# Performance work log

Hardware: AMD Instinct MI355X
Metric: run time of the kernel (lower is better)

## Reference

```python
import jax, jax.numpy as jnp
import numpy as np

B, S, D_MODEL = 2, 2048, 1024
H, D = 16, 64
D_INNER = H * D
EPS = 1e-5


def setup_inputs() -> dict:
    key = jax.random.key(0)
    ks = jax.random.split(key, 10)
    sc = 0.02
    return {
        "x": jax.random.normal(ks[0], (B, S, D_MODEL), dtype=jnp.float32),
        "Wq": jax.random.normal(ks[1], (D_MODEL, D_INNER), dtype=jnp.float32) * sc,
        "Wk": jax.random.normal(ks[2], (D_MODEL, D_INNER), dtype=jnp.float32) * sc,
        "Wv": jax.random.normal(ks[3], (D_MODEL, D_INNER), dtype=jnp.float32) * sc,
        "Wg": jax.random.normal(ks[4], (D_MODEL, D_INNER), dtype=jnp.float32) * sc,
        "Wa": jax.random.normal(ks[5], (D_MODEL, H), dtype=jnp.float32) * sc,
        "ba": jax.random.normal(ks[6], (H,), dtype=jnp.float32) * sc,
        "Wo": jax.random.normal(ks[7], (D_INNER, D_MODEL), dtype=jnp.float32) * sc,
        "gn_w": jnp.ones((D_INNER,), dtype=jnp.float32),
        "gn_b": jnp.zeros((D_INNER,), dtype=jnp.float32),
    }


def reference(x, Wq, Wk, Wv, Wg, Wa, ba, Wo, gn_w, gn_b):
    b, s, _ = x.shape
    # projections -> [B,H,S,D]
    q = jax.nn.silu(jnp.einsum('bsm,md->bsd', x, Wq).reshape(b, s, H, D).transpose(0, 2, 1, 3))
    k = jax.nn.silu(jnp.einsum('bsm,md->bsd', x, Wk).reshape(b, s, H, D).transpose(0, 2, 1, 3))
    v = jnp.einsum('bsm,md->bsd', x, Wv).reshape(b, s, H, D).transpose(0, 2, 1, 3)

    # data-dependent log forget gate, per head: [B,H,S]
    log_alpha = -jax.nn.softplus(jnp.einsum('bsm,mh->bsh', x, Wa) + ba)
    cum = jnp.cumsum(log_alpha, axis=1).transpose(0, 2, 1)  # [B,H,S]

    # decay[b,h,i,j] = exp(cum[i] - cum[j]) for j <= i, else 0
    diff = cum[:, :, :, None] - cum[:, :, None, :]  # [B,H,S,S]
    causal = jnp.tril(jnp.ones((s, s), dtype=bool))
    decay = jnp.exp(jnp.where(causal, diff, -jnp.inf))

    attn = jnp.einsum('bhid,bhjd->bhij', q, k) * decay
    o = jnp.einsum('bhij,bhjd->bhid', attn, v)  # [B,H,S,D]
    o = o.transpose(0, 2, 1, 3)  # [B,S,H,D]

    # GroupNorm(H groups) over channels-within-group and spatial dim S
    mean = jnp.mean(o, axis=(1, 3), keepdims=True)          # per (b,h)
    var = jnp.var(o, axis=(1, 3), keepdims=True)
    o = (o - mean) / jnp.sqrt(var + EPS)
    o = o * gn_w.reshape(H, D) + gn_b.reshape(H, D)
    o = o.reshape(b, s, H * D)

    gate = jax.nn.sigmoid(jnp.einsum('bsm,md->bsd', x, Wg))
    return jnp.einsum('bsd,dm->bsm', o * gate, Wo)
```

## Files before the change

kernel.cpp:

```cpp
#include <hip/hip_runtime.h>
#include <math.h>
#include <stdint.h>

typedef __attribute__((ext_vector_type(4))) float f32x4;
typedef __attribute__((ext_vector_type(8))) short bf16x8;

constexpr int NB = 2;
constexpr int NS = 2048;
constexpr int NM = 1024;
constexpr int NH = 16;
constexpr int ND = 64;
constexpr int NDI = 1024;

__device__ __forceinline__ float bf2f(unsigned short u) {
  uint32_t x = ((uint32_t)u) << 16; float f; __builtin_memcpy(&f, &x, 4); return f;
}
__device__ __forceinline__ unsigned short f2bf(float f) {
  uint32_t x; __builtin_memcpy(&x, &f, 4);
  x += 0x7FFFu + ((x >> 16) & 1u);
  return (unsigned short)(x >> 16);
}

__global__ __launch_bounds__(256) void k_cast_bf16(const float* __restrict__ in,
    unsigned short* __restrict__ out, int n8) {
  int i = blockIdx.x * 256 + threadIdx.x;
  if (i >= n8) return;
  const float4* p = (const float4*)(in + (size_t)i * 8);
  float4 a = p[0], b = p[1];
  unsigned short r[8] = {f2bf(a.x), f2bf(a.y), f2bf(a.z), f2bf(a.w),
                         f2bf(b.x), f2bf(b.y), f2bf(b.z), f2bf(b.w)};
  *(uint4*)(out + (size_t)i * 8) = *(const uint4*)r;
}

__global__ __launch_bounds__(256) void k_castT5(
    const float* __restrict__ w0, const float* __restrict__ w1,
    const float* __restrict__ w2, const float* __restrict__ w3,
    const float* __restrict__ w4,
    unsigned short* __restrict__ t0, unsigned short* __restrict__ t1,
    unsigned short* __restrict__ t2, unsigned short* __restrict__ t3,
    unsigned short* __restrict__ t4) {
  __shared__ float tile[32][33];
  int z = blockIdx.z;
  const float* src = z == 0 ? w0 : z == 1 ? w1 : z == 2 ? w2 : z == 3 ? w3 : w4;
  unsigned short* dst = z == 0 ? t0 : z == 1 ? t1 : z == 2 ? t2 : z == 3 ? t3 : t4;
  int c0 = blockIdx.x * 32, r0 = blockIdx.y * 32;
  int tx = threadIdx.x & 31, ty = threadIdx.x >> 5;
  #pragma unroll
  for (int i = 0; i < 4; i++)
    tile[ty + i * 8][tx] = src[(size_t)(r0 + ty + i * 8) * 1024 + c0 + tx];
  __syncthreads();
  #pragma unroll
  for (int i = 0; i < 4; i++)
    dst[(size_t)(c0 + ty + i * 8) * 1024 + r0 + tx] = f2bf(tile[tx][ty + i * 8]);
}

__global__ __launch_bounds__(256) void k_wa_fill(const float* __restrict__ Wa,
    unsigned short* __restrict__ wa_pad) {
  int idx = blockIdx.x * 256 + threadIdx.x;
  int h = idx >> 10, k2 = idx & 1023;
  wa_pad[idx] = (h < 16) ? f2bf(Wa[k2 * 16 + h]) : (unsigned short)0;
}

__global__ __launch_bounds__(256) void k_la_gemm(const unsigned short* __restrict__ xb,
    const unsigned short* __restrict__ wa_pad, float* __restrict__ la4) {
  __shared__ unsigned short As[128 * 32];
  __shared__ unsigned short Bs[128 * 32];
  int tid = threadIdx.x;
  int row0 = blockIdx.y * 128;
  int kbeg = blockIdx.x * 256;
  float* Cp = la4 + (size_t)blockIdx.x * (32 * 2048);
  int w = tid >> 6, l = tid & 63;
  int wr = w >> 1, wc = w & 1;
  int lr = l & 15, lk = l >> 4;
  f32x4 acc[4] = {};
  for (int k0 = kbeg; k0 < kbeg + 256; k0 += 32) {
    __syncthreads();
    #pragma unroll
    for (int i = 0; i < 2; i++) {
      int idx = tid + i * 256;
      int r = idx >> 2, c = idx & 3;
      int cs = c ^ ((r >> 1) & 3);
      const unsigned short* srcA = xb + (size_t)(row0 + r) * NM + k0 + cs * 8;
      const unsigned short* srcB = wa_pad + (size_t)r * NM + k0 + cs * 8;
      __builtin_amdgcn_global_load_lds(
          (const __attribute__((address_space(1))) void*)srcA,
          (__attribute__((address_space(3))) void*)((char*)As + (w * 64 + i * 256) * 16),
          16, 0, 0);
      __builtin_amdgcn_global_load_lds(
          (const __attribute__((address_space(1))) void*)srcB,
          (__attribute__((address_space(3))) void*)((char*)Bs + (w * 64 + i * 256) * 16),
          16, 0, 0);
    }
    __syncthreads();
    if (wc == 0) {
      bf16x8 b = *(const bf16x8*)&Bs[lr * 32 + (lk ^ ((lr >> 1) & 3)) * 8];
      #pragma unroll
      for (int m = 0; m < 4; m++) {
        int ra = wr * 64 + m * 16 + lr;
        bf16x8 a = *(const bf16x8*)&As[ra * 32 + (lk ^ ((ra >> 1) & 3)) * 8];
        acc[m] = __builtin_amdgcn_mfma_f32_16x16x32_bf16(a, b, acc[m], 0, 0, 0);
      }
    }
  }
  if (wc == 0) {
    #pragma unroll
    for (int m = 0; m < 4; m++) {
      #pragma unroll
      for (int j = 0; j < 4; j++) {
        int row = row0 + wr * 64 + m * 16 + lk * 4 + j;
        int bb = row >> 11, s = row & 2047;
        Cp[((size_t)(bb * 16 + lr)) * 2048 + s] = acc[m][j];
      }
    }
  }
}

__global__ __launch_bounds__(256) void k_cumsum(const float* __restrict__ la4,
    const float* __restrict__ ba, float* __restrict__ cum,
    float* __restrict__ psum, float* __restrict__ psq) {
  int g = blockIdx.x;
  int h = g & 15;
  if (threadIdx.x == 0) { psum[g] = 0.f; psq[g] = 0.f; }
  float bah = ba[h];
  const float* p0 = la4 + (size_t)g * NS;
  float* out = cum + (size_t)g * NS;
  __shared__ float part[256];
  float v[8]; float sum = 0.f;
  int base = threadIdx.x * 8;
  #pragma unroll
  for (int i = 0; i < 8; i++) {
    int s = base + i;
    float z = p0[s] + p0[65536 + s] + p0[131072 + s] + p0[196608 + s] + bah;
    float sp = fmaxf(z, 0.f) + log1pf(expf(-fabsf(z)));
    v[i] = -sp; sum += v[i];
  }
  part[threadIdx.x] = sum;
  __syncthreads();
  for (int off = 1; off < 256; off <<= 1) {
    float add = (threadIdx.x >= off) ? part[threadIdx.x - off] : 0.f;
    __syncthreads();
    part[threadIdx.x] += add;
    __syncthreads();
  }
  float run = (threadIdx.x > 0) ? part[threadIdx.x - 1] : 0.f;
  #pragma unroll
  for (int i = 0; i < 8; i++) { run += v[i]; out[base + i] = run; }
}

__global__ __launch_bounds__(512, 2) void k_proj8(
    const unsigned short* __restrict__ A,
    const unsigned short* __restrict__ Wcat,
    unsigned short* __restrict__ q, unsigned short* __restrict__ k,
    unsigned short* __restrict__ v, unsigned short* __restrict__ g) {
  __shared__ unsigned short Ab[2][256 * 64];
  __shared__ unsigned short Bb[2][256 * 64];
  int tid = threadIdx.x;
  int bid = blockIdx.x;
  int wg = (bid & 7) * 32 + (bid >> 3);
  int bx = wg & 15, by = wg >> 4;
  int row0 = by * 256, col0 = bx * 256;
  int wid = tid >> 6, lane = tid & 63;
  int WR = wid >> 2, WC = wid & 3;
  int lr = lane & 15, lk = lane >> 4;

  auto stage = [&](int kt, int bi) {
    #pragma unroll
    for (int i = 0; i < 4; i++) {
      int idx = tid + i * 512;
      int r = idx >> 3, c = idx & 7;
      int cs = c ^ (r & 7);
      const unsigned short* srcA = A + (size_t)(row0 + r) * NM + kt * 64 + cs * 8;
      __builtin_amdgcn_global_load_lds(
          (const __attribute__((address_space(1))) void*)srcA,
          (__attribute__((address_space(3))) void*)((char*)&Ab[bi][0] + (wid * 64 + i * 512) * 16),
          16, 0, 0);
      const unsigned short* srcB = Wcat + (size_t)(col0 + r) * NM + kt * 64 + cs * 8;
      __builtin_amdgcn_global_load_lds(
          (const __attribute__((address_space(1))) void*)srcB,
          (__attribute__((address_space(3))) void*)((char*)&Bb[bi][0] + (wid * 64 + i * 512) * 16),
          16, 0, 0);
    }
  };

  stage(0, 0);
  stage(1, 1);

  f32x4 acc[8][4] = {};
  for (int kt = 0; kt < 16; ++kt) {
    int bi = kt & 1;
    if (kt < 15) asm volatile("s_waitcnt vmcnt(8)" ::: "memory");
    else         asm volatile("s_waitcnt vmcnt(0)" ::: "memory");
    __builtin_amdgcn_sched_barrier(0);
    __builtin_amdgcn_s_barrier();

    const char* Ap = (const char*)&Ab[bi][0];
    const char* Bp = (const char*)&Bb[bi][0];
    bf16x8 a0[8], b0[4], a1[8], b1[4];
    #pragma unroll
    for (int m = 0; m < 8; m++) {
      int r = WR * 128 + m * 16 + lr;
      a0[m] = *(const bf16x8*)(Ap + r * 128 + ((lk ^ (r & 7)) * 16));
    }
    #pragma unroll
    for (int n = 0; n < 4; n++) {
      int r = WC * 64 + n * 16 + lr;
      b0[n] = *(const bf16x8*)(Bp + r * 128 + ((lk ^ (r & 7)) * 16));
    }
    #pragma unroll
    for (int m = 0; m < 8; m++)
      #pragma unroll
      for (int n = 0; n < 4; n++)
        acc[m][n] = __builtin_amdgcn_mfma_f32_16x16x32_bf16(a0[m], b0[n], acc[m][n], 0, 0, 0);
    #pragma unroll
    for (int m = 0; m < 8; m++) {
      int r = WR * 128 + m * 16 + lr;
      a1[m] = *(const bf16x8*)(Ap + r * 128 + (((lk + 4) ^ (r & 7)) * 16));
    }
    #pragma unroll
    for (int n = 0; n < 4; n++) {
      int r = WC * 64 + n * 16 + lr;
      b1[n] = *(const bf16x8*)(Bp + r * 128 + (((lk + 4) ^ (r & 7)) * 16));
    }
    asm volatile("s_waitcnt lgkmcnt(0)" ::: "memory");
    __builtin_amdgcn_sched_barrier(0);
    __builtin_amdgcn_s_barrier();
    if (kt + 2 < 16) stage(kt + 2, bi);
    __builtin_amdgcn_s_setprio(1);
    #pragma unroll
    for (int m = 0; m < 8; m++)
      #pragma unroll
      for (int n = 0; n < 4; n++)
        acc[m][n] = __builtin_amdgcn_mfma_f32_16x16x32_bf16(a1[m], b1[n], acc[m][n], 0, 0, 0);
    __builtin_amdgcn_s_setprio(0);
  }

  #pragma unroll
  for (int m = 0; m < 8; m++) {
    #pragma unroll
    for (int n = 0; n < 4; n++) {
      int col = col0 + WC * 64 + n * 16 + lr;
      int zone = col >> 10;
      unsigned short* dst = zone == 0 ? q : zone == 1 ? k : zone == 2 ? v : g;
      int cb = col & 1023;
      #pragma unroll
      for (int j = 0; j < 4; j++) {
        int row = row0 + WR * 128 + m * 16 + lk * 4 + j;
        float val = acc[m][n][j];
        if (zone <= 1) val = val / (1.f + expf(-val));
        else if (zone == 3) val = 1.f / (1.f + expf(-val));
        dst[(size_t)row * 1024 + cb] = f2bf(val);
      }
    }
  }
}

__global__ __launch_bounds__(256) void k_out2(const unsigned short* __restrict__ A,
    const unsigned short* __restrict__ Bt, float* __restrict__ C) {
  __shared__ unsigned short As[2][128 * 64];
  __shared__ unsigned short Bs[2][128 * 64];
  int tid = threadIdx.x;
  int bid = blockIdx.x;
  int wg = (bid & 7) * 32 + (bid >> 3);
  int bx = wg & 7, by = wg >> 3;
  int row0 = by * 128, col0 = bx * 128;
  int w = tid >> 6, l = tid & 63;
  int wr = w >> 1, wc = w & 1;
  int lr = l & 15, lk = l >> 4;

  auto stage = [&](int t, int bi) {
    #pragma unroll
    for (int i = 0; i < 4; i++) {
      int idx = tid + i * 256;
      int r = idx >> 3, c = idx & 7;
      int cs = c ^ (r & 7);
      const unsigned short* srcA = A + (size_t)(row0 + r) * NM + t * 64 + cs * 8;
      __builtin_amdgcn_global_load_lds(
          (const __attribute__((address_space(1))) void*)srcA,
          (__attribute__((address_space(3))) void*)((char*)&As[bi][0] + idx * 16),
          16, 0, 0);
      const unsigned short* srcB = Bt + (size_t)(col0 + r) * NM + t * 64 + cs * 8;
      __builtin_amdgcn_global_load_lds(
          (const __attribute__((address_space(1))) void*)srcB,
          (__attribute__((address_space(3))) void*)((char*)&Bs[bi][0] + idx * 16),
          16, 0, 0);
    }
  };

  stage(0, 0);
  asm volatile("s_waitcnt vmcnt(0)" ::: "memory");
  __builtin_amdgcn_s_barrier();

  f32x4 acc[4][4] = {};
  int cur = 0;
  for (int t = 0; t < 16; ++t) {
    if (t < 15) stage(t + 1, cur ^ 1);
    const char* Ap = (const char*)&As[cur][0];
    const char* Bp = (const char*)&Bs[cur][0];
    bf16x8 a[4][2], b[4][2];
    #pragma unroll
    for (int m = 0; m < 4; m++) {
      int ra = wr * 64 + m * 16 + lr;
      #pragma unroll
      for (int kk = 0; kk < 2; kk++)
        a[m][kk] = *(const bf16x8*)(Ap + ra * 128 + (((kk * 4 + lk) ^ (ra & 7)) * 16));
    }
    #pragma unroll
    for (int n = 0; n < 4; n++) {
      int rb = wc * 64 + n * 16 + lr;
      #pragma unroll
      for (int kk = 0; kk < 2; kk++)
        b[n][kk] = *(const bf16x8*)(Bp + rb * 128 + (((kk * 4 + lk) ^ (rb & 7)) * 16));
    }
    __builtin_amdgcn_s_setprio(1);
    #pragma unroll
    for (int kk = 0; kk < 2; kk++)
      #pragma unroll
      for (int m = 0; m < 4; m++)
        #pragma unroll
        for (int n = 0; n < 4; n++)
          acc[m][n] = __builtin_amdgcn_mfma_f32_16x16x32_bf16(a[m][kk], b[n][kk], acc[m][n], 0, 0, 0);
    __builtin_amdgcn_s_setprio(0);
    asm volatile("s_waitcnt vmcnt(0)" ::: "memory");
    __builtin_amdgcn_s_barrier();
    cur ^= 1;
  }
  #pragma unroll
  for (int m = 0; m < 4; m++)
    #pragma unroll
    for (int n = 0; n < 4; n++)
      #pragma unroll
      for (int j = 0; j < 4; j++) {
        int row = row0 + wr * 64 + m * 16 + lk * 4 + j;
        int col = col0 + wc * 64 + n * 16 + lr;
        C[(size_t)row * NM + col] = acc[m][n][j];
      }
}

__global__ __launch_bounds__(256) void k_attn(const unsigned short* __restrict__ q,
    const unsigned short* __restrict__ kk, const unsigned short* __restrict__ vv,
    const float* __restrict__ cum, float* __restrict__ o,
    float* __restrict__ psum, float* __restrict__ psq) {
  int it = blockIdx.x, h = blockIdx.y, b = blockIdx.z;
  int i0 = it * 64;
  __shared__ unsigned short Qs[64 * 64];
  __shared__ unsigned short Ks[64 * 64];
  __shared__ unsigned short Ps[64 * 64];
  __shared__ unsigned short Vs[64 * 66];
  __shared__ float ci[64], cj[64];
  __shared__ int jlo_s;
  int tid = threadIdx.x;
  int w = tid >> 6, lane = tid & 63;
  int cl = lane & 15, hi = lane >> 4;
  const size_t hb = (size_t)b * NS * NDI + (size_t)h * ND;
  const float* cumh = cum + (size_t)(b * NH + h) * NS;

  #pragma unroll
  for (int lp = 0; lp < 2; lp++) {
    int idx = tid + lp * 256;
    int r = idx >> 3, cb = (idx & 7) * 16;
    uint4 t = *(const uint4*)(q + hb + (size_t)(i0 + r) * NDI + (cb >> 1));
    *(uint4*)((char*)Qs + r * 128 + (cb ^ ((r & 7) << 4))) = t;
  }
  if (tid < 64) ci[tid] = cumh[i0 + tid];
  if (tid < 64) {
    int jt = tid;
    bool ok = (jt <= it) && (cumh[i0] - cumh[jt * 64 + 63] >= -60.f);
    unsigned long long mask = __ballot(ok);
    if (tid == 0) jlo_s = (int)__builtin_ctzll(mask);
  }
  __syncthreads();
  int jlo = jlo_s;

  int arow = w * 16 + cl;
  int xr = (cl & 7) << 4;
  const char* Qb = (const char*)Qs + arow * 128;
  const char* Pb = (const char*)Ps + arow * 128;
  f32x4 acco[4] = {};

  for (int jt = jlo; jt <= it; jt++) {
    int j0 = jt * 64;
    __syncthreads();
    if (tid < 64) cj[tid] = cumh[j0 + tid];
    __syncthreads();
    #pragma unroll
    for (int lp = 0; lp < 2; lp++) {
      int idx = tid + lp * 256;
      int r = idx >> 3, cb = (idx & 7) * 16;
      uint4 t = *(const uint4*)(kk + hb + (size_t)(j0 + r) * NDI + (cb >> 1));
      *(uint4*)((char*)Ks + r * 128 + (cb ^ ((r & 7) << 4))) = t;
      uint4 tv = *(const uint4*)(vv + hb + (size_t)(j0 + r) * NDI + (cb >> 1));
      unsigned int uv[4]; *(uint4*)uv = tv;
      unsigned int* vd = (unsigned int*)(Vs + r * 66 + (cb >> 1));
      vd[0] = uv[0]; vd[1] = uv[1]; vd[2] = uv[2]; vd[3] = uv[3];
    }
    __syncthreads();
    bf16x8 a0 = *(const bf16x8*)(Qb + ((hi * 16) ^ xr));
    bf16x8 a1 = *(const bf16x8*)(Qb + ((64 + hi * 16) ^ xr));
    f32x4 accs[4] = {};
    #pragma unroll
    for (int jtile = 0; jtile < 4; jtile++) {
      const char* Kb = (const char*)Ks + (jtile * 16 + cl) * 128;
      bf16x8 b0 = *(const bf16x8*)(Kb + ((hi * 16) ^ xr));
      bf16x8 b1 = *(const bf16x8*)(Kb + ((64 + hi * 16) ^ xr));
      accs[jtile] = __builtin_amdgcn_mfma_f32_16x16x32_bf16(a0, b0, accs[jtile], 0, 0, 0);
      accs[jtile] = __builtin_amdgcn_mfma_f32_16x16x32_bf16(a1, b1, accs[jtile], 0, 0, 0);
    }
    #pragma unroll
    for (int jtile = 0; jtile < 4; jtile++) {
      #pragma unroll
      for (int reg = 0; reg < 4; reg++) {
        int irl = w * 16 + hi * 4 + reg;
        int jl = jtile * 16 + cl;
        float dec = ((j0 + jl) <= (i0 + irl)) ? __expf(ci[irl] - cj[jl]) : 0.f;
        float pv = accs[jtile][reg] * dec;
        *(unsigned short*)((char*)Ps + irl * 128 + ((2 * jl) ^ ((irl & 7) << 4))) = f2bf(pv);
      }
    }
    __syncthreads();
    #pragma unroll
    for (int kk2 = 0; kk2 < 2; kk2++) {
      bf16x8 pa = *(const bf16x8*)(Pb + ((kk2 * 64 + hi * 16) ^ xr));
      #pragma unroll
      for (int dt = 0; dt < 4; dt++) {
        bf16x8 vb;
        #pragma unroll
        for (int e = 0; e < 8; e++)
          vb[e] = (short)Vs[(kk2 * 32 + hi * 8 + e) * 66 + dt * 16 + cl];
        acco[dt] = __builtin_amdgcn_mfma_f32_16x16x32_bf16(pa, vb, acco[dt], 0, 0, 0);
      }
    }
  }
  #pragma unroll
  for (int dt = 0; dt < 4; dt++) {
    #pragma unroll
    for (int reg = 0; reg < 4; reg++) {
      int row = i0 + w * 16 + hi * 4 + reg;
      o[hb + (size_t)row * NDI + dt * 16 + cl] = acco[dt][reg];
    }
  }
  __syncthreads();
  float* ls = (float*)Ps;
  float* lq = ls + 256;
  float sm = 0.f, sq = 0.f;
  #pragma unroll
  for (int dt = 0; dt < 4; dt++)
    #pragma unroll
    for (int reg = 0; reg < 4; reg++) { float t2 = acco[dt][reg]; sm += t2; sq += t2 * t2; }
  ls[tid] = sm; lq[tid] = sq;
  __syncthreads();
  for (int off = 128; off > 0; off >>= 1) {
    if (tid < off) { ls[tid] += ls[tid + off]; lq[tid] += lq[tid + off]; }
    __syncthreads();
  }
  if (tid == 0) {
    atomicAdd(&psum[b * NH + h], ls[0]);
    atomicAdd(&psq[b * NH + h], lq[0]);
  }
}

__global__ void k_gnfinal(const float* __restrict__ psum, const float* __restrict__ psq,
                          float* __restrict__ stats) {
  int g = threadIdx.x;
  if (g < 32) {
    float n = (float)(NS * ND);
    float mean = psum[g] / n;
    float var = psq[g] / n - mean * mean;
    stats[g * 2] = mean;
    stats[g * 2 + 1] = rsqrtf(var + 1e-5f);
  }
}

__global__ __launch_bounds__(256) void k_gate(const float* __restrict__ o,
    const unsigned short* __restrict__ gsig, const float* __restrict__ stats,
    const float* __restrict__ gnw, const float* __restrict__ gnb,
    unsigned short* __restrict__ u) {
  int idx4 = blockIdx.x * 256 + threadIdx.x;
  size_t base = (size_t)idx4 * 4;
  int c = (int)(base & (NDI - 1));
  int row = (int)(base >> 10);
  int b = row >> 11;
  int h = c >> 6;
  int g = b * NH + h;
  float mean = stats[g * 2], rstd = stats[g * 2 + 1];
  float4 ov = *(const float4*)(o + base);
  ushort4 gv = *(const ushort4*)(gsig + base);
  float4 w4 = *(const float4*)(gnw + c);
  float4 b4 = *(const float4*)(gnb + c);
  unsigned short r[4];
  r[0] = f2bf(((ov.x - mean) * rstd * w4.x + b4.x) * bf2f(gv.x));
  r[1] = f2bf(((ov.y - mean) * rstd * w4.y + b4.y) * bf2f(gv.y));
  r[2] = f2bf(((ov.z - mean) * rstd * w4.z + b4.z) * bf2f(gv.z));
  r[3] = f2bf(((ov.w - mean) * rstd * w4.w + b4.w) * bf2f(gv.w));
  *(ushort4*)(u + base) = *(const ushort4*)r;
}

extern "C" void kernel_launch(void* const* d_in, const int* in_sizes, int n_in,
                              void* d_out, int out_size, void* d_ws, size_t ws_size,
                              hipStream_t stream) {
  const float* x   = (const float*)d_in[0];
  const float* Wq  = (const float*)d_in[1];
  const float* Wk  = (const float*)d_in[2];
  const float* Wv  = (const float*)d_in[3];
  const float* Wg  = (const float*)d_in[4];
  const float* Wa  = (const float*)d_in[5];
  const float* ba  = (const float*)d_in[6];
  const float* Wo  = (const float*)d_in[7];
  const float* gnw = (const float*)d_in[8];
  const float* gnb = (const float*)d_in[9];
  float* out = (float*)d_out;

  const size_t NTOK = (size_t)NB * NS;
  char* p = (char*)d_ws;
  float* la4 = (float*)p;                 p += (size_t)4 * 32 * NS * 4;
  float* cum = (float*)p;                 p += (size_t)NB * NH * NS * 4;
  float* psum = (float*)p;                p += 32 * 4;
  float* psq  = (float*)p;                p += 32 * 4;
  float* stats = (float*)p;               p += 64 * 4;
  p = (char*)(((uintptr_t)p + 255) & ~(uintptr_t)255);
  unsigned short* xb   = (unsigned short*)p; p += NTOK * NM * 2;
  unsigned short* Wcat = (unsigned short*)p; p += (size_t)4 * NM * NDI * 2;
  unsigned short* wto  = (unsigned short*)p; p += (size_t)NDI * NM * 2;
  unsigned short* wa_pad = (unsigned short*)p; p += (size_t)128 * NM * 2;
  unsigned short* q  = (unsigned short*)p;  p += NTOK * NDI * 2;
  unsigned short* k  = (unsigned short*)p;  p += NTOK * NDI * 2;
  unsigned short* v  = (unsigned short*)p;  p += NTOK * NDI * 2;
  unsigned short* g  = (unsigned short*)p;  p += NTOK * NDI * 2;
  unsigned short* u  = (unsigned short*)p;  p += NTOK * NDI * 2;
  float* o = (float*)p;                     p += NTOK * NDI * 4;

  unsigned short* wtq = Wcat;
  unsigned short* wtk = Wcat + (size_t)NM * NDI;
  unsigned short* wtv = Wcat + (size_t)2 * NM * NDI;
  unsigned short* wtg = Wcat + (size_t)3 * NM * NDI;

  k_cast_bf16<<<dim3((int)(NTOK * NM / 8 / 256)), 256, 0, stream>>>(x, xb, (int)(NTOK * NM / 8));
  k_castT5   <<<dim3(32, 32, 5), 256, 0, stream>>>(Wq, Wk, Wv, Wg, Wo, wtq, wtk, wtv, wtg, wto);
  k_wa_fill  <<<dim3(512), 256, 0, stream>>>(Wa, wa_pad);
  k_la_gemm  <<<dim3(4, 32), 256, 0, stream>>>(xb, wa_pad, la4);
  k_cumsum   <<<dim3(NB * NH), 256, 0, stream>>>(la4, ba, cum, psum, psq);
  k_proj8    <<<dim3(256), 512, 0, stream>>>(xb, Wcat, q, k, v, g);
  k_attn     <<<dim3(32, NH, NB), 256, 0, stream>>>(q, k, v, cum, o, psum, psq);
  k_gnfinal  <<<1, 64, 0, stream>>>(psum, psq, stats);
  k_gate     <<<dim3(4096), 256, 0, stream>>>(o, g, stats, gnw, gnb, u);
  k_out2     <<<dim3(256), 256, 0, stream>>>(u, wto, out);
}
```

Before: 134.5 us.

## Merge prep kernels, reorder projection MFMA schedule, store attention output as bf16

Three prep kernels (x cast, weight transpose-casts, Wa pad) are folded into one launch, and the GroupNorm finalize kernel is dropped so the gate kernel computes mean and rstd inline. The attention output buffer becomes bf16 instead of fp32, which halves its write and read traffic. The projection GEMM inner loop is restructured into quadrant-ordered MFMA phases with smaller register fragments and extra barriers, and launch_bounds drops to one block per CU. These trade launch overhead and memory traffic for lower precision in the intermediate o and some risk of scheduling regressions in the projection GEMM.

```diff
diff --git a/kernel.cpp b/kernel.cpp
--- a/kernel.cpp
+++ b/kernel.cpp
@@ -21,44 +21,42 @@
   return (unsigned short)(x >> 16);
 }
 
-__global__ __launch_bounds__(256) void k_cast_bf16(const float* __restrict__ in,
-    unsigned short* __restrict__ out, int n8) {
-  int i = blockIdx.x * 256 + threadIdx.x;
-  if (i >= n8) return;
-  const float4* p = (const float4*)(in + (size_t)i * 8);
-  float4 a = p[0], b = p[1];
-  unsigned short r[8] = {f2bf(a.x), f2bf(a.y), f2bf(a.z), f2bf(a.w),
-                         f2bf(b.x), f2bf(b.y), f2bf(b.z), f2bf(b.w)};
-  *(uint4*)(out + (size_t)i * 8) = *(const uint4*)r;
-}
-
-__global__ __launch_bounds__(256) void k_castT5(
+__global__ __launch_bounds__(256) void k_prep(const float* __restrict__ x,
     const float* __restrict__ w0, const float* __restrict__ w1,
     const float* __restrict__ w2, const float* __restrict__ w3,
-    const float* __restrict__ w4,
+    const float* __restrict__ w4, const float* __restrict__ Wa,
+    unsigned short* __restrict__ xb,
     unsigned short* __restrict__ t0, unsigned short* __restrict__ t1,
     unsigned short* __restrict__ t2, unsigned short* __restrict__ t3,
-    unsigned short* __restrict__ t4) {
-  __shared__ float tile[32][33];
-  int z = blockIdx.z;
-  const float* src = z == 0 ? w0 : z == 1 ? w1 : z == 2 ? w2 : z == 3 ? w3 : w4;
-  unsigned short* dst = z == 0 ? t0 : z == 1 ? t1 : z == 2 ? t2 : z == 3 ? t3 : t4;
-  int c0 = blockIdx.x * 32, r0 = blockIdx.y * 32;
-  int tx = threadIdx.x & 31, ty = threadIdx.x >> 5;
-  #pragma unroll
-  for (int i = 0; i < 4; i++)
-    tile[ty + i * 8][tx] = src[(size_t)(r0 + ty + i * 8) * 1024 + c0 + tx];
-  __syncthreads();
-  #pragma unroll
-  for (int i = 0; i < 4; i++)
-    dst[(size_t)(c0 + ty + i * 8) * 1024 + r0 + tx] = f2bf(tile[tx][ty + i * 8]);
-}
-
-__global__ __launch_bounds__(256) void k_wa_fill(const float* __restrict__ Wa,
-    unsigned short* __restrict__ wa_pad) {
-  int idx = blockIdx.x * 256 + threadIdx.x;
-  int h = idx >> 10, k2 = idx & 1023;
-  wa_pad[idx] = (h < 16) ? f2bf(Wa[k2 * 16 + h]) : (unsigned short)0;
+    unsigned short* __restrict__ t4, unsigned short* __restrict__ wa_pad) {
+  int bid = blockIdx.x;
+  if (bid < 2048) {
+    int i = bid * 256 + threadIdx.x;
+    const float4* p = (const float4*)(x + (size_t)i * 8);
+    float4 a = p[0], b = p[1];
+    unsigned short r[8] = {f2bf(a.x), f2bf(a.y), f2bf(a.z), f2bf(a.w),
+                           f2bf(b.x), f2bf(b.y), f2bf(b.z), f2bf(b.w)};
+    *(uint4*)(xb + (size_t)i * 8) = *(const uint4*)r;
+  } else if (bid < 7168) {
+    __shared__ float tile[32][33];
+    int w = bid - 2048;
+    int z = w >> 10, within = w & 1023;
+    const float* src = z == 0 ? w0 : z == 1 ? w1 : z == 2 ? w2 : z == 3 ? w3 : w4;
+    unsigned short* dst = z == 0 ? t0 : z == 1 ? t1 : z == 2 ? t2 : z == 3 ? t3 : t4;
+    int c0 = (within & 31) * 32, r0 = (within >> 5) * 32;
+    int tx = threadIdx.x & 31, ty = threadIdx.x >> 5;
+    #pragma unroll
+    for (int i = 0; i < 4; i++)
+      tile[ty + i * 8][tx] = src[(size_t)(r0 + ty + i * 8) * 1024 + c0 + tx];
+    __syncthreads();
+    #pragma unroll
+    for (int i = 0; i < 4; i++)
+      dst[(size_t)(c0 + ty + i * 8) * 1024 + r0 + tx] = f2bf(tile[tx][ty + i * 8]);
+  } else {
+    int idx = (bid - 7168) * 256 + threadIdx.x;
+    int h = idx >> 10, k2 = idx & 1023;
+    wa_pad[idx] = (h < 16) ? f2bf(Wa[k2 * 16 + h]) : (unsigned short)0;
+  }
 }
 
 __global__ __launch_bounds__(256) void k_la_gemm(const unsigned short* __restrict__ xb,
@@ -147,7 +145,9 @@
   for (int i = 0; i < 8; i++) { run += v[i]; out[base + i] = run; }
 }
 
-__global__ __launch_bounds__(512, 2) void k_proj8(
+#define LD8(base, r, kc) (*(const bf16x8*)((base) + (size_t)(r) * 128 + ((((kc)) ^ ((r) & 7)) * 16)))
+
+__global__ __launch_bounds__(512, 1) void k_proj8(
     const unsigned short* __restrict__ A,
     const unsigned short* __restrict__ Wcat,
     unsigned short* __restrict__ q, unsigned short* __restrict__ k,
@@ -195,42 +195,68 @@
 
     const char* Ap = (const char*)&Ab[bi][0];
     const char* Bp = (const char*)&Bb[bi][0];
-    bf16x8 a0[8], b0[4], a1[8], b1[4];
-    #pragma unroll
-    for (int m = 0; m < 8; m++) {
+    bf16x8 a[4][2], blo[2][2], bhi[2][2];
+    #pragma unroll
+    for (int m = 0; m < 4; m++) {
       int r = WR * 128 + m * 16 + lr;
-      a0[m] = *(const bf16x8*)(Ap + r * 128 + ((lk ^ (r & 7)) * 16));
-    }
-    #pragma unroll
-    for (int n = 0; n < 4; n++) {
+      a[m][0] = LD8(Ap, r, lk); a[m][1] = LD8(Ap, r, lk + 4);
+    }
+    #pragma unroll
+    for (int n = 0; n < 2; n++) {
       int r = WC * 64 + n * 16 + lr;
-      b0[n] = *(const bf16x8*)(Bp + r * 128 + ((lk ^ (r & 7)) * 16));
-    }
-    #pragma unroll
-    for (int m = 0; m < 8; m++)
-      #pragma unroll
-      for (int n = 0; n < 4; n++)
-        acc[m][n] = __builtin_amdgcn_mfma_f32_16x16x32_bf16(a0[m], b0[n], acc[m][n], 0, 0, 0);
-    #pragma unroll
-    for (int m = 0; m < 8; m++) {
-      int r = WR * 128 + m * 16 + lr;
-      a1[m] = *(const bf16x8*)(Ap + r * 128 + (((lk + 4) ^ (r & 7)) * 16));
-    }
-    #pragma unroll
-    for (int n = 0; n < 4; n++) {
-      int r = WC * 64 + n * 16 + lr;
-      b1[n] = *(const bf16x8*)(Bp + r * 128 + (((lk + 4) ^ (r & 7)) * 16));
-    }
+      blo[n][0] = LD8(Bp, r, lk); blo[n][1] = LD8(Bp, r, lk + 4);
+    }
+    __builtin_amdgcn_s_setprio(1);
+    #pragma unroll
+    for (int kk = 0; kk < 2; kk++)
+      #pragma unroll
+      for (int m = 0; m < 4; m++)
+        #pragma unroll
+        for (int n = 0; n < 2; n++)
+          acc[m][n] = __builtin_amdgcn_mfma_f32_16x16x32_bf16(a[m][kk], blo[n][kk], acc[m][n], 0, 0, 0);
+    __builtin_amdgcn_s_setprio(0);
+    #pragma unroll
+    for (int n = 0; n < 2; n++) {
+      int r = WC * 64 + (2 + n) * 16 + lr;
+      bhi[n][0] = LD8(Bp, r, lk); bhi[n][1] = LD8(Bp, r, lk + 4);
+    }
+    __builtin_amdgcn_s_barrier();
+    __builtin_amdgcn_s_setprio(1);
+    #pragma unroll
+    for (int kk = 0; kk < 2; kk++)
+      #pragma unroll
+      for (int m = 0; m < 4; m++)
+        #pragma unroll
+        for (int n = 0; n < 2; n++)
+          acc[m][2 + n] = __builtin_amdgcn_mfma_f32_16x16x32_bf16(a[m][kk], bhi[n][kk], acc[m][2 + n], 0, 0, 0);
+    __builtin_amdgcn_s_setprio(0);
+    #pragma unroll
+    for (int m = 0; m < 4; m++) {
+      int r = WR * 128 + (4 + m) * 16 + lr;
+      a[m][0] = LD8(Ap, r, lk); a[m][1] = LD8(Ap, r, lk + 4);
+    }
+    __builtin_amdgcn_s_barrier();
+    __builtin_amdgcn_s_setprio(1);
+    #pragma unroll
+    for (int kk = 0; kk < 2; kk++)
+      #pragma unroll
+      for (int m = 0; m < 4; m++)
+        #pragma unroll
+        for (int n = 0; n < 2; n++)
+          acc[4 + m][2 + n] = __builtin_amdgcn_mfma_f32_16x16x32_bf16(a[m][kk], bhi[n][kk], acc[4 + m][2 + n], 0, 0, 0);
+    __builtin_amdgcn_s_setprio(0);
     asm volatile("s_waitcnt lgkmcnt(0)" ::: "memory");
     __builtin_amdgcn_sched_barrier(0);
     __builtin_amdgcn_s_barrier();
     if (kt + 2 < 16) stage(kt + 2, bi);
     __builtin_amdgcn_s_setprio(1);
     #pragma unroll
-    for (int m = 0; m < 8; m++)
-      #pragma unroll
-      for (int n = 0; n < 4; n++)
-        acc[m][n] = __builtin_amdgcn_mfma_f32_16x16x32_bf16(a1[m], b1[n], acc[m][n], 0, 0, 0);
+    for (int kk = 0; kk < 2; kk++)
+      #pragma unroll
+      for (int m = 0; m < 4; m++)
+        #pragma unroll
+        for (int n = 0; n < 2; n++)
+          acc[4 + m][n] = __builtin_amdgcn_mfma_f32_16x16x32_bf16(a[m][kk], blo[n][kk], acc[4 + m][n], 0, 0, 0);
     __builtin_amdgcn_s_setprio(0);
   }
 
@@ -338,7 +364,7 @@
 
 __global__ __launch_bounds__(256) void k_attn(const unsigned short* __restrict__ q,
     const unsigned short* __restrict__ kk, const unsigned short* __restrict__ vv,
-    const float* __restrict__ cum, float* __restrict__ o,
+    const float* __restrict__ cum, unsigned short* __restrict__ o,
     float* __restrict__ psum, float* __restrict__ psq) {
   int it = blockIdx.x, h = blockIdx.y, b = blockIdx.z;
   int i0 = it * 64;
@@ -435,7 +461,7 @@
     #pragma unroll
     for (int reg = 0; reg < 4; reg++) {
       int row = i0 + w * 16 + hi * 4 + reg;
-      o[hb + (size_t)row * NDI + dt * 16 + cl] = acco[dt][reg];
+      o[hb + (size_t)row * NDI + dt * 16 + cl] = f2bf(acco[dt][reg]);
     }
   }
   __syncthreads();
@@ -458,22 +484,10 @@
   }
 }
 
-__global__ void k_gnfinal(const float* __restrict__ psum, const float* __restrict__ psq,
-                          float* __restrict__ stats) {
-  int g = threadIdx.x;
-  if (g < 32) {
-    float n = (float)(NS * ND);
-    float mean = psum[g] / n;
-    float var = psq[g] / n - mean * mean;
-    stats[g * 2] = mean;
-    stats[g * 2 + 1] = rsqrtf(var + 1e-5f);
-  }
-}
-
-__global__ __launch_bounds__(256) void k_gate(const float* __restrict__ o,
-    const unsigned short* __restrict__ gsig, const float* __restrict__ stats,
-    const float* __restrict__ gnw, const float* __restrict__ gnb,
-    unsigned short* __restrict__ u) {
+__global__ __launch_bounds__(256) void k_gate(const unsigned short* __restrict__ o,
+    const unsigned short* __restrict__ gsig, const float* __restrict__ psum,
+    const float* __restrict__ psq, const float* __restrict__ gnw,
+    const float* __restrict__ gnb, unsigned short* __restrict__ u) {
   int idx4 = blockIdx.x * 256 + threadIdx.x;
   size_t base = (size_t)idx4 * 4;
   int c = (int)(base & (NDI - 1));
@@ -481,16 +495,19 @@
   int b = row >> 11;
   int h = c >> 6;
   int g = b * NH + h;
-  float mean = stats[g * 2], rstd = stats[g * 2 + 1];
-  float4 ov = *(const float4*)(o + base);
+  float n = (float)(NS * ND);
+  float mean = psum[g] / n;
+  float var = psq[g] / n - mean * mean;
+  float rstd = rsqrtf(var + 1e-5f);
+  ushort4 ov = *(const ushort4*)(o + base);
   ushort4 gv = *(const ushort4*)(gsig + base);
   float4 w4 = *(const float4*)(gnw + c);
   float4 b4 = *(const float4*)(gnb + c);
   unsigned short r[4];
-  r[0] = f2bf(((ov.x - mean) * rstd * w4.x + b4.x) * bf2f(gv.x));
-  r[1] = f2bf(((ov.y - mean) * rstd * w4.y + b4.y) * bf2f(gv.y));
-  r[2] = f2bf(((ov.z - mean) * rstd * w4.z + b4.z) * bf2f(gv.z));
-  r[3] = f2bf(((ov.w - mean) * rstd * w4.w + b4.w) * bf2f(gv.w));
+  r[0] = f2bf(((bf2f(ov.x) - mean) * rstd * w4.x + b4.x) * bf2f(gv.x));
+  r[1] = f2bf(((bf2f(ov.y) - mean) * rstd * w4.y + b4.y) * bf2f(gv.y));
+  r[2] = f2bf(((bf2f(ov.z) - mean) * rstd * w4.z + b4.z) * bf2f(gv.z));
+  r[3] = f2bf(((bf2f(ov.w) - mean) * rstd * w4.w + b4.w) * bf2f(gv.w));
   *(ushort4*)(u + base) = *(const ushort4*)r;
 }
 
@@ -515,7 +532,6 @@
   float* cum = (float*)p;                 p += (size_t)NB * NH * NS * 4;
   float* psum = (float*)p;                p += 32 * 4;
   float* psq  = (float*)p;                p += 32 * 4;
-  float* stats = (float*)p;               p += 64 * 4;
   p = (char*)(((uintptr_t)p + 255) & ~(uintptr_t)255);
   unsigned short* xb   = (unsigned short*)p; p += NTOK * NM * 2;
   unsigned short* Wcat = (unsigned short*)p; p += (size_t)4 * NM * NDI * 2;
@@ -526,21 +542,19 @@
   unsigned short* v  = (unsigned short*)p;  p += NTOK * NDI * 2;
   unsigned short* g  = (unsigned short*)p;  p += NTOK * NDI * 2;
   unsigned short* u  = (unsigned short*)p;  p += NTOK * NDI * 2;
-  float* o = (float*)p;                     p += NTOK * NDI * 4;
+  unsigned short* o  = (unsigned short*)p;  p += NTOK * NDI * 2;
 
   unsigned short* wtq = Wcat;
   unsigned short* wtk = Wcat + (size_t)NM * NDI;
   unsigned short* wtv = Wcat + (size_t)2 * NM * NDI;
   unsigned short* wtg = Wcat + (size_t)3 * NM * NDI;
 
-  k_cast_bf16<<<dim3((int)(NTOK * NM / 8 / 256)), 256, 0, stream>>>(x, xb, (int)(NTOK * NM / 8));
-  k_castT5   <<<dim3(32, 32, 5), 256, 0, stream>>>(Wq, Wk, Wv, Wg, Wo, wtq, wtk, wtv, wtg, wto);
-  k_wa_fill  <<<dim3(512), 256, 0, stream>>>(Wa, wa_pad);
-  k_la_gemm  <<<dim3(4, 32), 256, 0, stream>>>(xb, wa_pad, la4);
-  k_cumsum   <<<dim3(NB * NH), 256, 0, stream>>>(la4, ba, cum, psum, psq);
-  k_proj8    <<<dim3(256), 512, 0, stream>>>(xb, Wcat, q, k, v, g);
-  k_attn     <<<dim3(32, NH, NB), 256, 0, stream>>>(q, k, v, cum, o, psum, psq);
-  k_gnfinal  <<<1, 64, 0, stream>>>(psum, psq, stats);
-  k_gate     <<<dim3(4096), 256, 0, stream>>>(o, g, stats, gnw, gnb, u);
-  k_out2     <<<dim3(256), 256, 0, stream>>>(u, wto, out);
-}
+  k_prep    <<<dim3(7680), 256, 0, stream>>>(x, Wq, Wk, Wv, Wg, Wo, Wa,
+                                             xb, wtq, wtk, wtv, wtg, wto, wa_pad);
+  k_la_gemm <<<dim3(4, 32), 256, 0, stream>>>(xb, wa_pad, la4);
+  k_cumsum  <<<dim3(NB * NH), 256, 0, stream>>>(la4, ba, cum, psum, psq);
+  k_proj8   <<<dim3(256), 512, 0, stream>>>(xb, Wcat, q, k, v, g);
+  k_attn    <<<dim3(32, NH, NB), 256, 0, stream>>>(q, k, v, cum, o, psum, psq);
+  k_gate    <<<dim3(4096), 256, 0, stream>>>(o, g, psum, psq, gnw, gnb, u);
+  k_out2    <<<dim3(256), 256, 0, stream>>>(u, wto, out);
+}
```

Result: faster. 126.3 us (-6.1%).
